# Optimization experiments

Measured on AMD Instinct MI355X. Metric: run time of the kernel, lower is better.

The kernel has to match this reference:

```python
import jax, jax.numpy as jnp
import numpy as np

B, CIN, COUT, H, W = 4, 256, 256, 64, 64
KH, KW = 3, 3
STRIDE, PAD = 1, 1
K = KH * KW


def setup_inputs() -> dict:
    key = jax.random.key(0)
    k1, k2, k3 = jax.random.split(key, 3)
    x = jax.random.normal(k1, (B, CIN, H, W), dtype=jnp.float32)
    # small offset weights -> offsets of O(1) pixel, realistic near init
    offset_w = jax.random.normal(k2, (2 * K, CIN, KH, KW), dtype=jnp.float32) * 0.01
    offset_b = jnp.zeros((2 * K,), dtype=jnp.float32)
    dcn_w = jax.random.normal(k3, (COUT, CIN, KH, KW), dtype=jnp.float32) * (1.0 / np.sqrt(CIN * K))
    dcn_b = jnp.zeros((COUT,), dtype=jnp.float32)
    return {"x": x, "offset_w": offset_w, "offset_b": offset_b, "dcn_w": dcn_w, "dcn_b": dcn_b}


def _conv2d(x, w, b):
    y = jax.lax.conv_general_dilated(
        x, w, window_strides=(STRIDE, STRIDE),
        padding=((PAD, PAD), (PAD, PAD)),
        dimension_numbers=("NCHW", "OIHW", "NCHW"))
    return y + b[None, :, None, None]


def _bilinear_gather(x, py, px):
    """x: [B,C,H,W]; py,px: [B,K,Ho,Wo] float sample coords.
    Zero padding outside image (torchvision deform_conv2d semantics).
    Returns [B,C,K,Ho,Wo]."""
    Bb, C, Hin, Win = x.shape
    y0 = jnp.floor(py); x0 = jnp.floor(px)
    wy1 = py - y0; wx1 = px - x0
    y0i = y0.astype(jnp.int32); x0i = x0.astype(jnp.int32)
    x_flat = x.reshape(Bb, C, Hin * Win)

    def corner(yi, xi, wgt):
        valid = (yi >= 0) & (yi < Hin) & (xi >= 0) & (xi < Win)
        yc = jnp.clip(yi, 0, Hin - 1)
        xc = jnp.clip(xi, 0, Win - 1)
        idx = (yc * Win + xc).reshape(Bb, -1)  # [B, K*Ho*Wo]
        vals = jax.vmap(lambda xf, ix: jnp.take(xf, ix, axis=1))(x_flat, idx)
        vals = vals.reshape(Bb, C, *yi.shape[1:])  # [B,C,K,Ho,Wo]
        w_eff = jnp.where(valid, wgt, 0.0)[:, None]  # [B,1,K,Ho,Wo]
        return vals * w_eff

    out = corner(y0i, x0i, (1.0 - wy1) * (1.0 - wx1))
    out = out + corner(y0i, x0i + 1, (1.0 - wy1) * wx1)
    out = out + corner(y0i + 1, x0i, wy1 * (1.0 - wx1))
    out = out + corner(y0i + 1, x0i + 1, wy1 * wx1)
    return out


def _deformable_block(x, offset_w, offset_b, dcn_w, dcn_b):
    offset = _conv2d(x, offset_w, offset_b)  # [B, 2K, Ho, Wo]
    Bb, _, Ho, Wo = offset.shape
    off = offset.reshape(Bb, K, 2, Ho, Wo)
    dy, dx = off[:, :, 0], off[:, :, 1]  # torchvision: (y, x) interleaved per tap

    ky = jnp.repeat(jnp.arange(KH), KW).astype(jnp.float32)  # [K]
    kx = jnp.tile(jnp.arange(KW), KH).astype(jnp.float32)    # [K]
    base_y = (jnp.arange(Ho, dtype=jnp.float32) * STRIDE - PAD)[None, :, None] + ky[:, None, None]  # [K,Ho,1]
    base_x = (jnp.arange(Wo, dtype=jnp.float32) * STRIDE - PAD)[None, None, :] + kx[:, None, None]  # [K,1,Wo]
    py = base_y[None] + dy  # [B,K,Ho,Wo]
    px = base_x[None] + dx

    patches = _bilinear_gather(x, py, px)  # [B,C,K,Ho,Wo]
    wk = dcn_w.reshape(COUT, CIN, K)
    out = jnp.einsum("bckhw,ock->bohw", patches, wk)
    return out + dcn_b[None, :, None, None]


def reference(x, offset_w, offset_b, dcn_w, dcn_b):
    return _deformable_block(x, offset_w, offset_b, dcn_w, dcn_b)
```

## Files before the change

### kernel.cpp

```cpp
#include <hip/hip_runtime.h>

#define BB 4
#define CIN 256
#define COUT 256
#define HH 64
#define WW 64
#define KK 9
#define OC2 18
#define KTOT (CIN * KK)

typedef __attribute__((ext_vector_type(8))) _Float16 h8;
typedef __attribute__((ext_vector_type(4))) float f32x4;

static __device__ __forceinline__ h8 splat_pk(unsigned pk) {
    union { unsigned u[4]; h8 h; } s;
    s.u[0] = pk; s.u[1] = pk; s.u[2] = pk; s.u[3] = pk;
    return s.h;
}

__global__ __launch_bounds__(256) void prework_kernel(
    const float* __restrict__ x, const float* __restrict__ ow,
    const float* __restrict__ dw,
    _Float16* __restrict__ xT, _Float16* __restrict__ bp,
    _Float16* __restrict__ bow)
{
    const int bid = blockIdx.x;
    const int t = threadIdx.x;
    if (bid < 1024) {
        const int b = bid >> 8, y = (bid >> 2) & 63, c0 = (bid & 3) * 64;
        __shared__ float tile[64][65];
#pragma unroll
        for (int r = 0; r < 16; ++r) {
            int idx = r * 256 + t;
            int c = idx >> 6, w = idx & 63;
            tile[c][w] = x[(((size_t)(b * CIN + c0 + c)) << 12) + (y << 6) + w];
        }
        __syncthreads();
        const int px = t >> 2;
#pragma unroll
        for (int half = 0; half < 2; ++half) {
            int cc = (t & 3) + half * 4;
            union { _Float16 h[8]; uint4 q; } u;
#pragma unroll
            for (int j = 0; j < 8; ++j) u.h[j] = (_Float16)tile[cc * 8 + j][px];
            size_t el = (((size_t)(b << 12)) + (y << 6) + px) * 256 + c0 + cc * 8;
            *(uint4*)&xT[el] = u.q;
        }
    } else if (bid < 1312) {
        int wid = (bid - 1024) * 256 + t;
        int T = wid >> 10;
        int r = wid & 1023;
        int cotile = r >> 6, lane = r & 63;
        int co = cotile * 16 + (lane & 15);
        int kbase = T * 32 + ((lane >> 4) & 3) * 8;
        union { _Float16 h[8]; uint4 q; } u;
#pragma unroll
        for (int j = 0; j < 8; ++j) {
            int k = kbase + j;
            int c = k & 255, kk = k >> 8;
            u.h[j] = (_Float16)dw[co * KTOT + c * KK + kk];
        }
        *(uint4*)&bp[(size_t)wid * 8] = u.q;
    } else {
        int wid = (bid - 1312) * 256 + t;
        int T = wid >> 7;
        int r = wid & 127;
        int lane = r & 63;
        int oc = ((r >> 6) << 4) + (lane & 15);
        int kbase = T * 32 + ((lane >> 4) & 3) * 8;
        union { _Float16 h[8]; uint4 q; } u;
#pragma unroll
        for (int j = 0; j < 8; ++j) {
            int k = kbase + j;
            int c = k & 255, kk = k >> 8;
            u.h[j] = (oc < OC2) ? (_Float16)ow[oc * KTOT + c * KK + kk] : (_Float16)0.f;
        }
        *(uint4*)&bow[(size_t)wid * 8] = u.q;
    }
}

__global__ __launch_bounds__(512) void offset_mfma_kernel(
    const _Float16* __restrict__ xT, const _Float16* __restrict__ bow,
    float* __restrict__ opart)
{
    const int bid = blockIdx.x;
    const int m_blk = bid >> 1, kh = bid & 1;
    const int b = m_blk >> 5;
    const int pxbase = (m_blk & 31) * 128;
    const int tid = threadIdx.x;
    const int lane = tid & 63, wv = tid >> 6;
    const int colg = lane & 15, kg = lane >> 4;

    const int pxl = pxbase + (wv << 4) + colg;
    const int py = pxl >> 6, pxx = pxl & 63;

    const _Float16* xb = xT + ((size_t)b << 20);

    auto GLOAD = [&](int T, h8& R) {
        int kk = T >> 3;
        int ky = kk / 3, kx = kk - 3 * (kk / 3);
        int yy = py + ky - 1, xx = pxx + kx - 1;
        h8 v = {0, 0, 0, 0, 0, 0, 0, 0};
        if ((unsigned)yy < HH && (unsigned)xx < WW)
            v = *(const h8*)(xb + ((((yy << 6) + xx) << 8) + ((T & 7) << 5) + (kg << 3)));
        R = v;
    };
    auto BLOAD = [&](int T, uint4* br) {
#pragma unroll
        for (int nj = 0; nj < 2; ++nj)
            br[nj] = *(const uint4*)&bow[(size_t)(((T << 1) + nj) * 64 + lane) * 8];
    };

    f32x4 acc[2];
    { f32x4 z = {0.f, 0.f, 0.f, 0.f}; acc[0] = z; acc[1] = z; }

    const int Tb = kh * 36;
    h8 E, F;
    uint4 bA[2], bB[2];

    GLOAD(Tb, E);
    BLOAD(Tb, bA);
    for (int r = 0; r < 36; r += 2) {
        GLOAD(Tb + r + 1, F);
        BLOAD(Tb + r + 1, bB);
        {
            union { uint4 q; h8 h; } u0, u1;
            u0.q = bA[0]; u1.q = bA[1];
            acc[0] = __builtin_amdgcn_mfma_f32_16x16x32_f16(E, u0.h, acc[0], 0, 0, 0);
            acc[1] = __builtin_amdgcn_mfma_f32_16x16x32_f16(E, u1.h, acc[1], 0, 0, 0);
        }
        if (r + 2 < 36) { GLOAD(Tb + r + 2, E); BLOAD(Tb + r + 2, bA); }
        {
            union { uint4 q; h8 h; } u0, u1;
            u0.q = bB[0]; u1.q = bB[1];
            acc[0] = __builtin_amdgcn_mfma_f32_16x16x32_f16(F, u0.h, acc[0], 0, 0, 0);
            acc[1] = __builtin_amdgcn_mfma_f32_16x16x32_f16(F, u1.h, acc[1], 0, 0, 0);
        }
    }

    const int pxb = pxbase + (wv << 4) + kg * 4;
#pragma unroll
    for (int nj = 0; nj < 2; ++nj) {
        int oc = nj * 16 + colg;
        if (oc < OC2) {
            float4 o;
            o.x = acc[nj][0]; o.y = acc[nj][1];
            o.z = acc[nj][2]; o.w = acc[nj][3];
            *(float4*)&opart[(((size_t)((kh * BB + b) * OC2 + oc)) << 12) + pxb] = o;
        }
    }
}

__global__ __launch_bounds__(512, 4) void dcn_mfma_kernel(
    const _Float16* __restrict__ xT, const float* __restrict__ opart,
    const float* __restrict__ ob, const _Float16* __restrict__ bp,
    const float* __restrict__ db, float* __restrict__ out)
{
    __shared__ __align__(16) _Float16 Asl[2][512 * 8];
    __shared__ __align__(8) uint2 twp[288];
    __shared__ __align__(8) uint2 tih[288];

    int P = blockIdx.x;
    int L = (P & 7) * 64 + (P >> 3);
    const int b = L >> 7;
    const int rowbase = (L & 127) * 32;

    const int tid = threadIdx.x;
    const int lane = tid & 63;
    const int wn = tid >> 6;
    const int colg = lane & 15, kg = lane >> 4;

    const int g_px = tid >> 4;
    const int g_cg = tid & 15;
    const int g_ebase = g_px * 9;
    const int g_w0 = g_cg * 32 + (g_px ^ (g_cg & 7));

    const float* op0 = opart + (((size_t)(b * OC2)) << 12);
    const float* op1 = opart + (((size_t)((BB + b) * OC2)) << 12);
    if (tid < 288) {
        int e = tid;
        int p = e / 9, kk = e - (e / 9) * 9;
        int pxl = rowbase + p;
        int y = pxl >> 6, xx = pxl & 63;
        float dy = op0[((size_t)(2 * kk) << 12) + pxl]
                 + op1[((size_t)(2 * kk) << 12) + pxl] + ob[2 * kk];
        float dx = op0[((size_t)(2 * kk + 1) << 12) + pxl]
                 + op1[((size_t)(2 * kk + 1) << 12) + pxl] + ob[2 * kk + 1];
        int ky = kk / 3, kx = kk - 3 * (kk / 3);
        float sy = (float)(y - 1 + ky) + dy;
        float sx = (float)(xx - 1 + kx) + dx;
        float fy = floorf(sy), fx = floorf(sx);
        int y0 = (int)fy, x0 = (int)fx;
        float wy1 = sy - fy, wx1 = sx - fx;
        float wy0 = 1.f - wy1, wx0 = 1.f - wx1;
        bool vy0 = (unsigned)y0 < HH, vy1 = (unsigned)(y0 + 1) < HH;
        bool vx0 = (unsigned)x0 < WW, vx1 = (unsigned)(x0 + 1) < WW;
        _Float16 w00 = (_Float16)((vy0 && vx0) ? wy0 * wx0 : 0.f);
        _Float16 w01 = (_Float16)((vy0 && vx1) ? wy0 * wx1 : 0.f);
        _Float16 w10 = (_Float16)((vy1 && vx0) ? wy1 * wx0 : 0.f);
        _Float16 w11 = (_Float16)((vy1 && vx1) ? wy1 * wx1 : 0.f);
        union { _Float16 h[2]; unsigned u; } pk2;
        uint2 W;
        pk2.h[0] = w00; pk2.h[1] = w01; W.x = pk2.u;
        pk2.h[0] = w10; pk2.h[1] = w11; W.y = pk2.u;
        twp[e] = W;
        int y0c = min(max(y0, 0), HH - 1), y1c = min(max(y0 + 1, 0), HH - 1);
        int x0c = min(max(x0, 0), WW - 1), x1c = min(max(x0 + 1, 0), WW - 1);
        unsigned i00 = (unsigned)((y0c << 6) + x0c);
        unsigned i01 = (unsigned)((y0c << 6) + x1c);
        unsigned i10 = (unsigned)((y1c << 6) + x0c);
        unsigned i11 = (unsigned)((y1c << 6) + x1c);
        tih[e] = make_uint2(i00 | (i01 << 16), i10 | (i11 << 16));
    }
    __syncthreads();

    const char* xbyte = (const char*)(xT + ((size_t)b << 20));

    auto AGLOAD = [&](int st, h8* C) {
        uint2 ij = tih[g_ebase + (st >> 1)];
        unsigned chb = (unsigned)((st & 1) * 256 + g_cg * 16);
        C[0] = *(const h8*)(xbyte + (((ij.x & 0xFFFFu) << 9) + chb));
        C[1] = *(const h8*)(xbyte + (((ij.x >> 16)     << 9) + chb));
        C[2] = *(const h8*)(xbyte + (((ij.y & 0xFFFFu) << 9) + chb));
        C[3] = *(const h8*)(xbyte + (((ij.y >> 16)     << 9) + chb));
    };
    auto GCONSUME = [&](int st, int buf, const h8* C) {
        uint2 w = twp[g_ebase + (st >> 1)];
        unsigned w00 = (w.x & 0xFFFFu) * 0x10001u;
        unsigned w01 = (w.x >> 16)     * 0x10001u;
        unsigned w10 = (w.y & 0xFFFFu) * 0x10001u;
        unsigned w11 = (w.y >> 16)     * 0x10001u;
        h8 v = C[0] * splat_pk(w00);
        v += C[1] * splat_pk(w01);
        v += C[2] * splat_pk(w10);
        v += C[3] * splat_pk(w11);
        *(h8*)&Asl[buf][g_w0 * 8] = v;
    };
    auto BLOAD = [&](int st, uint4* br) {
#pragma unroll
        for (int ks = 0; ks < 4; ++ks)
#pragma unroll
            for (int nj = 0; nj < 2; ++nj) {
                size_t word = ((size_t)((st * 4 + ks) * 16 + wn * 2 + nj)) * 64 + lane;
                br[ks * 2 + nj] = *(const uint4*)&bp[word * 8];
            }
    };

    f32x4 acc[2][2];
#pragma unroll
    for (int mi = 0; mi < 2; ++mi)
#pragma unroll
        for (int nj = 0; nj < 2; ++nj) { f32x4 z = {0.f,0.f,0.f,0.f}; acc[mi][nj] = z; }

    auto MFMA16 = [&](int buf, uint4* br) {
        __builtin_amdgcn_s_setprio(1);
#pragma unroll
        for (int ks = 0; ks < 4; ++ks) {
            const int cg = ks * 4 + kg;
            union { uint4 q; h8 h; } b0, b1;
            b0.q = br[ks * 2]; b1.q = br[ks * 2 + 1];
#pragma unroll
            for (int mi = 0; mi < 2; ++mi) {
                int w = cg * 32 + ((mi * 16 + colg) ^ (cg & 7));
                h8 a = *(const h8*)&Asl[buf][w * 8];
                acc[mi][0] = __builtin_amdgcn_mfma_f32_16x16x32_f16(a, b0.h, acc[mi][0], 0, 0, 0);
                acc[mi][1] = __builtin_amdgcn_mfma_f32_16x16x32_f16(a, b1.h, acc[mi][1], 0, 0, 0);
            }
        }
        __builtin_amdgcn_s_setprio(0);
    };

    h8 C[4];
    uint4 breg[8], bnext[8];

    AGLOAD(0, C);
    BLOAD(0, breg);
    GCONSUME(0, 0, C);
    __syncthreads();

    for (int s = 0; s < 18; ++s) {
        const int cur = s & 1;
        if (s + 1 < 18) {
            AGLOAD(s + 1, C);
            BLOAD(s + 1, bnext);
        }
        MFMA16(cur, breg);
        if (s + 1 < 18) GCONSUME(s + 1, cur ^ 1, C);
        __syncthreads();
#pragma unroll
        for (int i = 0; i < 8; ++i) breg[i] = bnext[i];
    }

#pragma unroll
    for (int nj = 0; nj < 2; ++nj) {
        const int co = wn * 32 + nj * 16 + colg;
        const float bv = db[co];
        float* op = out + ((size_t)(b * COUT + co) << 12) + rowbase + kg * 4;
#pragma unroll
        for (int mi = 0; mi < 2; ++mi) {
            float4 o;
            o.x = acc[mi][nj][0] + bv;
            o.y = acc[mi][nj][1] + bv;
            o.z = acc[mi][nj][2] + bv;
            o.w = acc[mi][nj][3] + bv;
            *(float4*)&op[mi * 16] = o;
        }
    }
}

extern "C" void kernel_launch(void* const* d_in, const int* in_sizes, int n_in,
                              void* d_out, int out_size, void* d_ws, size_t ws_size,
                              hipStream_t stream)
{
    const float* x  = (const float*)d_in[0];
    const float* ow = (const float*)d_in[1];
    const float* ob = (const float*)d_in[2];
    const float* dw = (const float*)d_in[3];
    const float* db = (const float*)d_in[4];
    float* out = (float*)d_out;

    char* wsp = (char*)d_ws;
    float*     opart = (float*)wsp;
    _Float16*  bp    = (_Float16*)(wsp + 2359296);
    _Float16*  bow   = (_Float16*)(wsp + 3538944);
    _Float16*  xT    = (_Float16*)(wsp + 3686400);

    hipLaunchKernelGGL(prework_kernel,     dim3(1348), dim3(256), 0, stream, x, ow, dw, xT, bp, bow);
    hipLaunchKernelGGL(offset_mfma_kernel, dim3(256),  dim3(512), 0, stream, xT, bow, opart);
    hipLaunchKernelGGL(dcn_mfma_kernel,    dim3(512),  dim3(512), 0, stream, xT, opart, ob, bp, db, out);
}
```

Before: 70.66 us.

## Fuse offset convolution into DCN kernel, computing offsets per block in LDS

```diff
diff --git a/kernel.cpp b/kernel.cpp
--- a/kernel.cpp
+++ b/kernel.cpp
@@ -79,86 +79,16 @@
     }
 }
 
-__global__ __launch_bounds__(512) void offset_mfma_kernel(
+__global__ __launch_bounds__(512, 4) void dcn_mfma_kernel(
     const _Float16* __restrict__ xT, const _Float16* __restrict__ bow,
-    float* __restrict__ opart)
-{
-    const int bid = blockIdx.x;
-    const int m_blk = bid >> 1, kh = bid & 1;
-    const int b = m_blk >> 5;
-    const int pxbase = (m_blk & 31) * 128;
-    const int tid = threadIdx.x;
-    const int lane = tid & 63, wv = tid >> 6;
-    const int colg = lane & 15, kg = lane >> 4;
-
-    const int pxl = pxbase + (wv << 4) + colg;
-    const int py = pxl >> 6, pxx = pxl & 63;
-
-    const _Float16* xb = xT + ((size_t)b << 20);
-
-    auto GLOAD = [&](int T, h8& R) {
-        int kk = T >> 3;
-        int ky = kk / 3, kx = kk - 3 * (kk / 3);
-        int yy = py + ky - 1, xx = pxx + kx - 1;
-        h8 v = {0, 0, 0, 0, 0, 0, 0, 0};
-        if ((unsigned)yy < HH && (unsigned)xx < WW)
-            v = *(const h8*)(xb + ((((yy << 6) + xx) << 8) + ((T & 7) << 5) + (kg << 3)));
-        R = v;
-    };
-    auto BLOAD = [&](int T, uint4* br) {
-#pragma unroll
-        for (int nj = 0; nj < 2; ++nj)
-            br[nj] = *(const uint4*)&bow[(size_t)(((T << 1) + nj) * 64 + lane) * 8];
-    };
-
-    f32x4 acc[2];
-    { f32x4 z = {0.f, 0.f, 0.f, 0.f}; acc[0] = z; acc[1] = z; }
-
-    const int Tb = kh * 36;
-    h8 E, F;
-    uint4 bA[2], bB[2];
-
-    GLOAD(Tb, E);
-    BLOAD(Tb, bA);
-    for (int r = 0; r < 36; r += 2) {
-        GLOAD(Tb + r + 1, F);
-        BLOAD(Tb + r + 1, bB);
-        {
-            union { uint4 q; h8 h; } u0, u1;
-            u0.q = bA[0]; u1.q = bA[1];
-            acc[0] = __builtin_amdgcn_mfma_f32_16x16x32_f16(E, u0.h, acc[0], 0, 0, 0);
-            acc[1] = __builtin_amdgcn_mfma_f32_16x16x32_f16(E, u1.h, acc[1], 0, 0, 0);
-        }
-        if (r + 2 < 36) { GLOAD(Tb + r + 2, E); BLOAD(Tb + r + 2, bA); }
-        {
-            union { uint4 q; h8 h; } u0, u1;
-            u0.q = bB[0]; u1.q = bB[1];
-            acc[0] = __builtin_amdgcn_mfma_f32_16x16x32_f16(F, u0.h, acc[0], 0, 0, 0);
-            acc[1] = __builtin_amdgcn_mfma_f32_16x16x32_f16(F, u1.h, acc[1], 0, 0, 0);
-        }
-    }
-
-    const int pxb = pxbase + (wv << 4) + kg * 4;
-#pragma unroll
-    for (int nj = 0; nj < 2; ++nj) {
-        int oc = nj * 16 + colg;
-        if (oc < OC2) {
-            float4 o;
-            o.x = acc[nj][0]; o.y = acc[nj][1];
-            o.z = acc[nj][2]; o.w = acc[nj][3];
-            *(float4*)&opart[(((size_t)((kh * BB + b) * OC2 + oc)) << 12) + pxb] = o;
-        }
-    }
-}
-
-__global__ __launch_bounds__(512, 4) void dcn_mfma_kernel(
-    const _Float16* __restrict__ xT, const float* __restrict__ opart,
     const float* __restrict__ ob, const _Float16* __restrict__ bp,
     const float* __restrict__ db, float* __restrict__ out)
 {
-    __shared__ __align__(16) _Float16 Asl[2][512 * 8];
-    __shared__ __align__(8) uint2 twp[288];
-    __shared__ __align__(8) uint2 tih[288];
+    __shared__ __align__(16) char smem[32768 + 4608 + 4608];
+    _Float16 (*Asl)[4096] = (_Float16(*)[4096])smem;
+    float* oscr = (float*)smem;
+    uint2* twp = (uint2*)(smem + 32768);
+    uint2* tih = (uint2*)(smem + 32768 + 4608);
 
     int P = blockIdx.x;
     int L = (P & 7) * 64 + (P >> 3);
@@ -170,22 +100,67 @@
     const int wn = tid >> 6;
     const int colg = lane & 15, kg = lane >> 4;
 
-    const int g_px = tid >> 4;
-    const int g_cg = tid & 15;
-    const int g_ebase = g_px * 9;
-    const int g_w0 = g_cg * 32 + (g_px ^ (g_cg & 7));
-
-    const float* op0 = opart + (((size_t)(b * OC2)) << 12);
-    const float* op1 = opart + (((size_t)((BB + b) * OC2)) << 12);
+    const char* xbyte = (const char*)(xT + ((size_t)b << 20));
+
+    {
+        f32x4 oacc[2][2];
+#pragma unroll
+        for (int mi = 0; mi < 2; ++mi)
+#pragma unroll
+            for (int nj = 0; nj < 2; ++nj) { f32x4 z = {0.f,0.f,0.f,0.f}; oacc[mi][nj] = z; }
+
+        const int T0 = wn * 9;
+#pragma unroll
+        for (int i = 0; i < 9; ++i) {
+            int T = T0 + i;
+            int kk = T >> 3;
+            int ky = kk / 3, kx = kk - 3 * (kk / 3);
+            int cgo = ((T & 7) << 2) + kg;
+            h8 a[2];
+#pragma unroll
+            for (int mi = 0; mi < 2; ++mi) {
+                int pxl = rowbase + mi * 16 + colg;
+                int yy = (pxl >> 6) + ky - 1, xx = (pxl & 63) + kx - 1;
+                h8 v = {0,0,0,0,0,0,0,0};
+                if ((unsigned)yy < HH && (unsigned)xx < WW)
+                    v = *(const h8*)(xbyte + ((((yy << 6) + xx) << 9) + (cgo << 4)));
+                a[mi] = v;
+            }
+            union { uint4 q; h8 h; } bw[2];
+#pragma unroll
+            for (int nj = 0; nj < 2; ++nj)
+                bw[nj].q = *(const uint4*)&bow[(size_t)(((T << 1) + nj) * 64 + lane) * 8];
+#pragma unroll
+            for (int mi = 0; mi < 2; ++mi)
+#pragma unroll
+                for (int nj = 0; nj < 2; ++nj)
+                    oacc[mi][nj] = __builtin_amdgcn_mfma_f32_16x16x32_f16(
+                        a[mi], bw[nj].h, oacc[mi][nj], 0, 0, 0);
+        }
+#pragma unroll
+        for (int mi = 0; mi < 2; ++mi)
+#pragma unroll
+            for (int nj = 0; nj < 2; ++nj) {
+                int px0 = mi * 16 + kg * 4;
+                int oc = nj * 16 + colg;
+#pragma unroll
+                for (int r = 0; r < 4; ++r)
+                    oscr[(wn * 32 + px0 + r) * 32 + oc] = oacc[mi][nj][r];
+            }
+    }
+    __syncthreads();
+
     if (tid < 288) {
         int e = tid;
         int p = e / 9, kk = e - (e / 9) * 9;
+        float dy = ob[2 * kk], dx = ob[2 * kk + 1];
+#pragma unroll
+        for (int w2 = 0; w2 < 8; ++w2) {
+            dy += oscr[(w2 * 32 + p) * 32 + 2 * kk];
+            dx += oscr[(w2 * 32 + p) * 32 + 2 * kk + 1];
+        }
         int pxl = rowbase + p;
         int y = pxl >> 6, xx = pxl & 63;
-        float dy = op0[((size_t)(2 * kk) << 12) + pxl]
-                 + op1[((size_t)(2 * kk) << 12) + pxl] + ob[2 * kk];
-        float dx = op0[((size_t)(2 * kk + 1) << 12) + pxl]
-                 + op1[((size_t)(2 * kk + 1) << 12) + pxl] + ob[2 * kk + 1];
         int ky = kk / 3, kx = kk - 3 * (kk / 3);
         float sy = (float)(y - 1 + ky) + dy;
         float sx = (float)(xx - 1 + kx) + dx;
@@ -214,7 +189,10 @@
     }
     __syncthreads();
 
-    const char* xbyte = (const char*)(xT + ((size_t)b << 20));
+    const int g_px = tid >> 4;
+    const int g_cg = tid & 15;
+    const int g_ebase = g_px * 9;
+    const int g_w0 = g_cg * 32 + (g_px ^ (g_cg & 7));
 
     auto AGLOAD = [&](int st, h8* C) {
         uint2 ij = tih[g_ebase + (st >> 1)];
@@ -320,12 +298,10 @@
     float* out = (float*)d_out;
 
     char* wsp = (char*)d_ws;
-    float*     opart = (float*)wsp;
-    _Float16*  bp    = (_Float16*)(wsp + 2359296);
-    _Float16*  bow   = (_Float16*)(wsp + 3538944);
-    _Float16*  xT    = (_Float16*)(wsp + 3686400);
-
-    hipLaunchKernelGGL(prework_kernel,     dim3(1348), dim3(256), 0, stream, x, ow, dw, xT, bp, bow);
-    hipLaunchKernelGGL(offset_mfma_kernel, dim3(256),  dim3(512), 0, stream, xT, bow, opart);
-    hipLaunchKernelGGL(dcn_mfma_kernel,    dim3(512),  dim3(512), 0, stream, xT, opart, ob, bp, db, out);
+    _Float16*  bp  = (_Float16*)wsp;
+    _Float16*  bow = (_Float16*)(wsp + 1179648);
+    _Float16*  xT  = (_Float16*)(wsp + 1327104);
+
+    hipLaunchKernelGGL(prework_kernel,  dim3(1348), dim3(256), 0, stream, x, ow, dw, xT, bp, bow);
+    hipLaunchKernelGGL(dcn_mfma_kernel, dim3(512),  dim3(512), 0, stream, xT, bow, ob, bp, db, out);
 }
```

New measurement: 63.43 us. 10.2% less time.
